# Performance work log

Hardware: AMD Instinct MI355X
Metric: run time of the kernel (lower is better)

The kernel has to match this reference:

```python
import jax, jax.numpy as jnp
import numpy as np

VOCAB = 20000
E = 300      # word embedding size (GloVe)
H = 1024     # n_hidden
G = 8        # n_head
N_OUT = 300  # output GloVe-space dim
N_ANS = 4000 # answer candidates
B, NQ, NK = 64, 32, 256


def setup_inputs() -> dict:
    key = jax.random.key(0)
    ks = jax.random.split(key, 12)
    s = lambda fan_in: 1.0 / np.sqrt(fan_in)
    return {
        "he_ques": jax.random.randint(ks[0], (B, NQ), 0, VOCAB),
        "he_kg": jax.random.randint(ks[1], (B, NK), 0, VOCAB),
        "emb": jax.random.normal(ks[2], (VOCAB, E), dtype=jnp.float32),
        "Wq": jax.random.normal(ks[3], (E, H), dtype=jnp.float32) * s(E),
        "bq": jnp.zeros((H,), dtype=jnp.float32),
        "Wk": jax.random.normal(ks[4], (E, H), dtype=jnp.float32) * s(E),
        "bk": jnp.zeros((H,), dtype=jnp.float32),
        "Watt": jax.random.normal(ks[5], (H, G), dtype=jnp.float32) * s(H),
        "batt": jnp.zeros((G,), dtype=jnp.float32),
        "Wout": jax.random.normal(ks[6], (H * G, N_OUT), dtype=jnp.float32) * s(H * G),
        "bout": jnp.zeros((N_OUT,), dtype=jnp.float32),
        "glove_cands": jax.random.normal(ks[7], (N_ANS, N_OUT), dtype=jnp.float32),
    }


def reference(he_ques, he_kg, emb, Wq, bq, Wk, bk, Watt, batt, Wout, bout, glove_cands):
    # Embed + project (dropout p=0 at eval)
    hq = emb[he_ques] @ Wq + bq          # [B, NQ, H]
    hk = emb[he_kg] @ Wk + bk            # [B, NK, H]
    # Attention logits: original builds outer product [B,NQ,NK,H] then Linear(H->G).
    # Fused as a single bilinear contraction (same math, no huge intermediate).
    logits = jnp.einsum('bqd,bkd,dg->bgqk', hq, hk, Watt) + batt[None, :, None, None]
    b, g, nq, nk = logits.shape
    att = jax.nn.softmax(logits.reshape(b, g, nq * nk), axis=2).reshape(b, g, nq, nk)
    # Per-head bilinear pooling: out[b,g,d] = sum_{q,k} hq[b,q,d] * att[b,g,q,k] * hk[b,k,d]
    pooled = jnp.einsum('bqd,bgqk,bkd->bgd', hq, att, hk)  # [B, G, H]
    out = pooled.reshape(b, g * hq.shape[-1]) @ Wout + bout  # [B, N_OUT]
    sim = out @ glove_cands.T                                # [B, N_ANS]
    return jax.nn.log_softmax(sim, axis=1)
```

## Files before the change

kernel.cpp:

```cpp
#include <hip/hip_runtime.h>
#include <math.h>

#define VOCAB 20000
#define E     300
#define EP    320
#define H     1024
#define G     8
#define NOUT  300
#define NP    320
#define KOUT  8192
#define NANS  4000
#define B     64
#define NQ    32
#define NK    256

typedef __attribute__((ext_vector_type(8))) short bf16x8;
typedef __attribute__((ext_vector_type(4))) float f32x4;

__device__ inline ushort f2bf(float x) {
    union { float f; unsigned u; } c; c.f = x;
    unsigned r = c.u + 0x7FFF + ((c.u >> 16) & 1);
    return (ushort)(r >> 16);
}
__device__ inline float bf2f(ushort x) {
    union { unsigned u; float f; } c; c.u = ((unsigned)x) << 16;
    return c.f;
}
#define MFMA(a, b, c) __builtin_amdgcn_mfma_f32_16x16x32_bf16((a), (b), (c), 0, 0, 0)

__global__ __launch_bounds__(256) void prep_emb(
    const float* __restrict__ emb, ushort* __restrict__ emb_bf)
{
    const int r0 = blockIdx.x * 64;
    for (int i = threadIdx.x; i < 64 * 80; i += 256) {
        int r = r0 + (i / 80), c = i % 80;
        if (r >= VOCAB) break;
        ushort4 o{0, 0, 0, 0};
        if (c < 75) {
            float4 v = *(const float4*)(emb + (long)r * E + c * 4);
            o.x = f2bf(v.x); o.y = f2bf(v.y); o.z = f2bf(v.z); o.w = f2bf(v.w);
        }
        *(ushort4*)(emb_bf + (long)r * EP + c * 4) = o;
    }
}

__global__ __launch_bounds__(256) void prep_wt(
    const float* __restrict__ Wq, const float* __restrict__ Wk,
    ushort* __restrict__ WTq, ushort* __restrict__ WTk)
{
    const float* W = blockIdx.z ? Wk : Wq;
    ushort* WT = blockIdx.z ? WTk : WTq;
    const int h0 = blockIdx.x * 64;
    const int e0 = blockIdx.y * 64;
    __shared__ float lf[64][65];
    const int t = threadIdx.x;

    for (int i = t; i < 64 * 64; i += 256) {
        int ec = i >> 6, hh = i & 63;
        int e = e0 + ec;
        lf[hh][ec] = (e < E) ? W[(long)e * H + h0 + hh] : 0.f;
    }
    __syncthreads();
    for (int i = t; i < 64 * 16; i += 256) {
        int hh = i >> 4, c = i & 15;
        ushort4 o;
        o.x = f2bf(lf[hh][c * 4 + 0]);
        o.y = f2bf(lf[hh][c * 4 + 1]);
        o.z = f2bf(lf[hh][c * 4 + 2]);
        o.w = f2bf(lf[hh][c * 4 + 3]);
        *(ushort4*)(WT + (long)(h0 + hh) * EP + e0 + c * 4) = o;
    }
}

__global__ __launch_bounds__(256) void prep_woutT(
    const float* __restrict__ Wout, ushort* __restrict__ woutT)
{
    const int k0 = blockIdx.x * 64, n0 = blockIdx.y * 64;
    __shared__ ushort td[64][72];
    for (int i = threadIdx.x; i < 64 * 64; i += 256) {
        int kk = i >> 6, nn = i & 63;
        int n = n0 + nn;
        float v = (n < NOUT) ? Wout[(k0 + kk) * NOUT + n] : 0.f;
        td[nn][kk] = f2bf(v);
    }
    __syncthreads();
    for (int i = threadIdx.x; i < 64 * 8; i += 256) {
        int nn = i >> 3, c = i & 7;
        *(bf16x8*)(woutT + (n0 + nn) * KOUT + k0 + c * 8) =
            *(const bf16x8*)(&td[nn][c * 8]);
    }
}

template <int WRITE_T>
__global__ __launch_bounds__(256, 2) void proj_big(
    const int* __restrict__ idx, const ushort* __restrict__ emb_bf,
    const ushort* __restrict__ WT, const float* __restrict__ bias,
    ushort* __restrict__ outr, ushort* __restrict__ outT)
{
    __shared__ ushort lds[128 * 130];
    __shared__ int sidx[128];
    const int r0 = blockIdx.x * 128;
    const int n0 = blockIdx.y * 128;
    const int t = threadIdx.x;

    if (t < 128) sidx[t] = idx[r0 + t];

    const int w = t >> 6, l = t & 63, lr = l & 15, lc = l >> 4;
    const int wm = (w >> 1) * 64, wn = (w & 1) * 64;
    const int srow = t >> 2;
    const int scol = (t & 3) * 8;
    ushort* As = lds;
    ushort* Bs = lds + 5120;
    f32x4 acc[4][4] = {};

    __syncthreads();

    for (int kk = 0; kk < 10; ++kk) {
        if (kk) __syncthreads();
        #pragma unroll
        for (int p = 0; p < 2; ++p) {
            int r = p * 64 + srow;
            *(bf16x8*)(As + r * 40 + scol) =
                *(const bf16x8*)(emb_bf + (long)sidx[r] * EP + kk * 32 + scol);
            *(bf16x8*)(Bs + r * 40 + scol) =
                *(const bf16x8*)(WT + (long)(n0 + r) * EP + kk * 32 + scol);
        }
        __syncthreads();

        bf16x8 af[4], bf[4];
        #pragma unroll
        for (int mf = 0; mf < 4; ++mf)
            af[mf] = *(const bf16x8*)(As + (wm + mf * 16 + lr) * 40 + lc * 8);
        #pragma unroll
        for (int nf = 0; nf < 4; ++nf)
            bf[nf] = *(const bf16x8*)(Bs + (wn + nf * 16 + lr) * 40 + lc * 8);
        #pragma unroll
        for (int mf = 0; mf < 4; ++mf)
            #pragma unroll
            for (int nf = 0; nf < 4; ++nf)
                acc[mf][nf] = MFMA(af[mf], bf[nf], acc[mf][nf]);
    }
    __syncthreads();

    #pragma unroll
    for (int mf = 0; mf < 4; ++mf)
    #pragma unroll
    for (int nf = 0; nf < 4; ++nf) {
        const int col = wn + nf * 16 + lr;
        const float bv = bias[n0 + col];
        #pragma unroll
        for (int r = 0; r < 4; ++r)
            lds[(wm + mf * 16 + lc * 4 + r) * 130 + col] =
                f2bf(acc[mf][nf][r] + bv);
    }
    __syncthreads();

    for (int i = t; i < 128 * 16; i += 256) {
        int k = i >> 4, c = i & 15;
        *(bf16x8*)(outr + (long)(r0 + k) * H + n0 + c * 8) =
            *(const bf16x8*)(lds + k * 130 + c * 8);
    }
    if (WRITE_T) {
        const int b = r0 >> 8, k0 = r0 & 255;
        for (int i = t; i < 128 * 16; i += 256) {
            int d = i >> 4, c = i & 15;
            ushort tmp[8];
            #pragma unroll
            for (int j = 0; j < 8; ++j) tmp[j] = lds[(c * 8 + j) * 130 + d];
            *(bf16x8*)(outT + (long)b * (H * NK) + (n0 + d) * NK + k0 + c * 8) =
                *(const bf16x8*)(tmp);
        }
    }
}

__global__ __launch_bounds__(512) void attn_mfma(
    const ushort* __restrict__ hq, const ushort* __restrict__ hk,
    const float* __restrict__ watt, const float* __restrict__ batt,
    ushort* __restrict__ att)
{
    const int b = blockIdx.x, g = blockIdx.y;
    const int t = threadIdx.x, w = t >> 6, l = t & 63, lr = l & 15, lc = l >> 4;
    __shared__ float wg[H];
    __shared__ ushort As[32 * 72];
    __shared__ ushort Bs[256 * 72];
    __shared__ float red[16];

    for (int i = t; i < H; i += 512) wg[i] = watt[i * G + g];

    f32x4 acc[2][2] = {};
    __syncthreads();

    for (int kk = 0; kk < 16; ++kk) {
        if (kk) __syncthreads();
        if (t < 256) {
            int r = t >> 3, c8 = (t & 7) * 8;
            bf16x8 hv = *(const bf16x8*)(hq + (b * NQ + r) * H + kk * 64 + c8);
            bf16x8 o;
            #pragma unroll
            for (int j = 0; j < 8; ++j)
                o[j] = (short)f2bf(bf2f((ushort)hv[j]) * wg[kk * 64 + c8 + j]);
            *(bf16x8*)(As + r * 72 + c8) = o;
        }
        #pragma unroll
        for (int p = 0; p < 4; ++p) {
            int j = t + 512 * p;
            int r = j >> 3, c8 = (j & 7) * 8;
            *(bf16x8*)(Bs + r * 72 + c8) =
                *(const bf16x8*)(hk + (b * NK + r) * H + kk * 64 + c8);
        }
        __syncthreads();

        #pragma unroll
        for (int ks = 0; ks < 2; ++ks) {
            bf16x8 a0 = *(const bf16x8*)(As + lr * 72 + ks * 32 + lc * 8);
            bf16x8 a1 = *(const bf16x8*)(As + (16 + lr) * 72 + ks * 32 + lc * 8);
            bf16x8 b0 = *(const bf16x8*)(Bs + (w * 32 + lr) * 72 + ks * 32 + lc * 8);
            bf16x8 b1 = *(const bf16x8*)(Bs + (w * 32 + 16 + lr) * 72 + ks * 32 + lc * 8);
            acc[0][0] = MFMA(a0, b0, acc[0][0]);
            acc[0][1] = MFMA(a0, b1, acc[0][1]);
            acc[1][0] = MFMA(a1, b0, acc[1][0]);
            acc[1][1] = MFMA(a1, b1, acc[1][1]);
        }
    }

    const float bg = batt[g];
    float lm = -1e30f;
    #pragma unroll
    for (int mt = 0; mt < 2; ++mt)
    #pragma unroll
    for (int nf = 0; nf < 2; ++nf)
    #pragma unroll
    for (int r = 0; r < 4; ++r) {
        acc[mt][nf][r] += bg;
        lm = fmaxf(lm, acc[mt][nf][r]);
    }
    #pragma unroll
    for (int off = 32; off; off >>= 1) lm = fmaxf(lm, __shfl_xor(lm, off));
    if (l == 0) red[w] = lm;
    __syncthreads();
    float gm = red[0];
    #pragma unroll
    for (int i = 1; i < 8; ++i) gm = fmaxf(gm, red[i]);

    float ls = 0.f;
    #pragma unroll
    for (int mt = 0; mt < 2; ++mt)
    #pragma unroll
    for (int nf = 0; nf < 2; ++nf)
    #pragma unroll
    for (int r = 0; r < 4; ++r) {
        float e = __expf(acc[mt][nf][r] - gm);
        acc[mt][nf][r] = e;
        ls += e;
    }
    #pragma unroll
    for (int off = 32; off; off >>= 1) ls += __shfl_xor(ls, off);
    if (l == 0) red[8 + w] = ls;
    __syncthreads();
    float sum = red[8];
    #pragma unroll
    for (int i = 9; i < 16; ++i) sum += red[i];
    const float inv = 1.f / sum;

    ushort* op = att + (b * 8 + g) * (NQ * NK);
    #pragma unroll
    for (int mt = 0; mt < 2; ++mt)
    #pragma unroll
    for (int nf = 0; nf < 2; ++nf)
    #pragma unroll
    for (int r = 0; r < 4; ++r)
        op[(mt * 16 + lc * 4 + r) * NK + w * 32 + nf * 16 + lr] =
            f2bf(acc[mt][nf][r] * inv);
}

__global__ __launch_bounds__(256, 2) void pooled_big(
    const ushort* __restrict__ att, const ushort* __restrict__ hkT,
    const ushort* __restrict__ hq, ushort* __restrict__ pooled_bf)
{
    __shared__ ushort lds[128 * 80];
    const int b = blockIdx.x, mt = blockIdx.y, nt = blockIdx.z;
    const int t = threadIdx.x;
    const int w = t >> 6, l = t & 63, lr = l & 15, lc = l >> 4;
    const int wm = (w >> 1) * 64, wn = (w & 1) * 64;
    const int srow = t >> 2;
    const int scol = (t & 3) * 8;
    ushort* As = lds;
    ushort* Bs = lds + 5120;
    const ushort* ab = att + (long)b * (G * NQ * NK) + (long)mt * 128 * NK;
    const ushort* bb = hkT + (long)b * (H * NK) + (long)nt * 128 * NK;
    f32x4 acc[4][4] = {};

    for (int kk = 0; kk < 8; ++kk) {
        if (kk) __syncthreads();
        #pragma unroll
        for (int p = 0; p < 2; ++p) {
            int r = p * 64 + srow;
            *(bf16x8*)(As + r * 40 + scol) =
                *(const bf16x8*)(ab + (long)r * NK + kk * 32 + scol);
            *(bf16x8*)(Bs + r * 40 + scol) =
                *(const bf16x8*)(bb + (long)r * NK + kk * 32 + scol);
        }
        __syncthreads();

        bf16x8 af[4], bf[4];
        #pragma unroll
        for (int mf = 0; mf < 4; ++mf)
            af[mf] = *(const bf16x8*)(As + (wm + mf * 16 + lr) * 40 + lc * 8);
        #pragma unroll
        for (int nf = 0; nf < 4; ++nf)
            bf[nf] = *(const bf16x8*)(Bs + (wn + nf * 16 + lr) * 40 + lc * 8);
        #pragma unroll
        for (int mf = 0; mf < 4; ++mf)
            #pragma unroll
            for (int nf = 0; nf < 4; ++nf)
                acc[mf][nf] = MFMA(af[mf], bf[nf], acc[mf][nf]);
    }
    __syncthreads();

    for (int i = t; i < 32 * 16; i += 256) {
        int r = i >> 4, c8 = (i & 15) * 8;
        *(bf16x8*)(lds + r * 136 + c8) =
            *(const bf16x8*)(hq + ((long)b * NQ + r) * H + nt * 128 + c8);
    }
    __syncthreads();

    float s[2][4] = {};
    #pragma unroll
    for (int nf = 0; nf < 4; ++nf) {
        const int col = wn + nf * 16 + lr;
        #pragma unroll
        for (int mf = 0; mf < 4; ++mf) {
            #pragma unroll
            for (int r = 0; r < 4; ++r) {
                const int q = (wm + mf * 16 + lc * 4 + r) & 31;
                s[mf >> 1][nf] += acc[mf][nf][r] * bf2f(lds[q * 136 + col]);
            }
        }
    }
    #pragma unroll
    for (int gl = 0; gl < 2; ++gl)
    #pragma unroll
    for (int nf = 0; nf < 4; ++nf) {
        float v = s[gl][nf];
        v += __shfl_xor(v, 16);
        v += __shfl_xor(v, 32);
        if (l < 16) {
            const int g = mt * 4 + (wm >> 5) + gl;
            const int d = nt * 128 + wn + nf * 16 + lr;
            pooled_bf[((long)b * G + g) * H + d] = f2bf(v);
        }
    }
}

__global__ __launch_bounds__(256) void outproj_mfma(
    const ushort* __restrict__ pooled_bf, const ushort* __restrict__ woutT,
    float* __restrict__ partial)
{
    const int ks = blockIdx.x;
    const int k0 = ks * 128;
    const int t = threadIdx.x, w = t >> 6, l = t & 63, lr = l & 15, lc = l >> 4;
    const ushort* ap = pooled_bf + lr * KOUT + k0 + lc * 8;
    const ushort* bp = woutT + (w * 80 + lr) * KOUT + k0 + lc * 8;
    f32x4 acc[4][5] = {};

    #pragma unroll
    for (int kk = 0; kk < 4; ++kk) {
        bf16x8 a[4];
        #pragma unroll
        for (int mt = 0; mt < 4; ++mt)
            a[mt] = *(const bf16x8*)(ap + mt * 16 * KOUT + kk * 32);
        #pragma unroll
        for (int nt = 0; nt < 5; ++nt) {
            bf16x8 bfr = *(const bf16x8*)(bp + nt * 16 * KOUT + kk * 32);
            #pragma unroll
            for (int mt = 0; mt < 4; ++mt)
                acc[mt][nt] = MFMA(a[mt], bfr, acc[mt][nt]);
        }
    }

    #pragma unroll
    for (int mt = 0; mt < 4; ++mt)
    #pragma unroll
    for (int nt = 0; nt < 5; ++nt)
    #pragma unroll
    for (int r = 0; r < 4; ++r) {
        const int bb = mt * 16 + lc * 4 + r;
        const int n = w * 80 + nt * 16 + lr;
        partial[(ks * B + bb) * NP + n] = acc[mt][nt][r];
    }
}

__global__ __launch_bounds__(256) void reduce_out_kernel(
    const float* __restrict__ partial, const float* __restrict__ bout,
    float* __restrict__ outv)
{
    const int i = blockIdx.x * 256 + threadIdx.x;
    if (i >= B * 304) return;
    const int b = i / 304, n = i % 304;
    float acc = 0.f;
    if (n < NOUT) {
        acc = bout[n];
        for (int ks = 0; ks < 64; ++ks)
            acc += partial[(ks * B + b) * NP + n];
    }
    outv[b * 304 + n] = acc;
}

__global__ __launch_bounds__(256) void sim_kernel(
    const float* __restrict__ outv, const float* __restrict__ glove,
    float* __restrict__ sim)
{
    __shared__ __align__(16) float ov[64][308];
    __shared__ __align__(16) float gl[16][308];
    const int t = threadIdx.x;
    const int a0 = blockIdx.x * 16;

    for (int i = t; i < 64 * 75; i += 256) {
        int r = i / 75, c = i % 75;
        *(float4*)(&ov[r][c * 4]) = *(const float4*)(&outv[r * 304 + c * 4]);
    }
    for (int i = t; i < 16 * 75; i += 256) {
        int r = i / 75, c = i % 75;
        *(float4*)(&gl[r][c * 4]) = *(const float4*)(&glove[(a0 + r) * NOUT + c * 4]);
    }
    __syncthreads();

    const int a = t & 15, bg = t >> 4;
    float acc[4] = {};
    for (int k4 = 0; k4 < 75; ++k4) {
        float4 g = *(const float4*)(&gl[a][k4 * 4]);
        #pragma unroll
        for (int bi = 0; bi < 4; ++bi) {
            float4 o = *(const float4*)(&ov[bg * 4 + bi][k4 * 4]);
            acc[bi] += g.x * o.x + g.y * o.y + g.z * o.z + g.w * o.w;
        }
    }
    #pragma unroll
    for (int bi = 0; bi < 4; ++bi)
        sim[(bg * 4 + bi) * NANS + a0 + a] = acc[bi];
}

__global__ __launch_bounds__(256) void lsm_kernel(
    const float* __restrict__ sim, float* __restrict__ dout)
{
    const int b = blockIdx.x, t = threadIdx.x;
    const float* p = sim + b * NANS;
    __shared__ float red[4];

    float4 v[4];
    float lm = -1e30f;
    #pragma unroll
    for (int j = 0; j < 4; ++j) {
        int i = t + j * 256;
        if (i < 1000) {
            v[j] = ((const float4*)p)[i];
            lm = fmaxf(lm, fmaxf(fmaxf(v[j].x, v[j].y), fmaxf(v[j].z, v[j].w)));
        }
    }
    #pragma unroll
    for (int off = 32; off; off >>= 1) lm = fmaxf(lm, __shfl_xor(lm, off));
    if ((t & 63) == 0) red[t >> 6] = lm;
    __syncthreads();
    const float gm = fmaxf(fmaxf(red[0], red[1]), fmaxf(red[2], red[3]));

    float ls = 0.f;
    #pragma unroll
    for (int j = 0; j < 4; ++j) {
        int i = t + j * 256;
        if (i < 1000)
            ls += __expf(v[j].x - gm) + __expf(v[j].y - gm) +
                  __expf(v[j].z - gm) + __expf(v[j].w - gm);
    }
    #pragma unroll
    for (int off = 32; off; off >>= 1) ls += __shfl_xor(ls, off);
    __syncthreads();
    if ((t & 63) == 0) red[t >> 6] = ls;
    __syncthreads();
    const float sh = gm + logf(red[0] + red[1] + red[2] + red[3]);

    #pragma unroll
    for (int j = 0; j < 4; ++j) {
        int i = t + j * 256;
        if (i < 1000) {
            float4 o;
            o.x = v[j].x - sh; o.y = v[j].y - sh;
            o.z = v[j].z - sh; o.w = v[j].w - sh;
            ((float4*)(dout + b * NANS))[i] = o;
        }
    }
}

extern "C" void kernel_launch(void* const* d_in, const int* in_sizes, int n_in,
                              void* d_out, int out_size, void* d_ws, size_t ws_size,
                              hipStream_t stream)
{
    (void)in_sizes; (void)n_in; (void)out_size; (void)ws_size;
    const int*   he_q  = (const int*)  d_in[0];
    const int*   he_k  = (const int*)  d_in[1];
    const float* emb   = (const float*)d_in[2];
    const float* Wq    = (const float*)d_in[3];
    const float* bq    = (const float*)d_in[4];
    const float* Wk    = (const float*)d_in[5];
    const float* bk    = (const float*)d_in[6];
    const float* Watt  = (const float*)d_in[7];
    const float* batt  = (const float*)d_in[8];
    const float* Wout  = (const float*)d_in[9];
    const float* bout  = (const float*)d_in[10];
    const float* glove = (const float*)d_in[11];
    float* out = (float*)d_out;

    ushort* WTq    = (ushort*)d_ws;
    ushort* WTk    = WTq + 327680;
    ushort* emb_bf = WTk + 327680;
    ushort* hq_bf  = emb_bf + 6400000;
    ushort* hk_bf  = hq_bf + 2097152;
    ushort* hkT    = hk_bf + 16777216;
    ushort* pool_bf= hkT + 16777216;
    ushort* woutT  = pool_bf + 524288;
    ushort* att    = woutT + 2621440;
    float*  partial= (float*)(att + 4194304);
    float*  outv   = partial + 1310720;
    float*  sim    = outv + 19456;

    prep_emb<<<dim3(313), 256, 0, stream>>>(emb, emb_bf);
    prep_wt<<<dim3(16, 5, 2), 256, 0, stream>>>(Wq, Wk, WTq, WTk);
    prep_woutT<<<dim3(128, 5), 256, 0, stream>>>(Wout, woutT);
    proj_big<0><<<dim3(16, 8), 256, 0, stream>>>(he_q, emb_bf, WTq, bq, hq_bf, nullptr);
    proj_big<1><<<dim3(128, 8), 256, 0, stream>>>(he_k, emb_bf, WTk, bk, hk_bf, hkT);
    attn_mfma<<<dim3(64, 8), 512, 0, stream>>>(hq_bf, hk_bf, Watt, batt, att);
    pooled_big<<<dim3(64, 2, 8), 256, 0, stream>>>(att, hkT, hq_bf, pool_bf);
    outproj_mfma<<<dim3(64), 256, 0, stream>>>(pool_bf, woutT, partial);
    reduce_out_kernel<<<dim3(76), 256, 0, stream>>>(partial, bout, outv);
    sim_kernel<<<dim3(250), 256, 0, stream>>>(outv, glove, sim);
    lsm_kernel<<<dim3(64), 256, 0, stream>>>(sim, out);
}
```

Before: 138.9 us.

## Gather fp32 embeddings directly in projection and merge prep/projection launches

```diff
diff --git a/kernel.cpp b/kernel.cpp
--- a/kernel.cpp
+++ b/kernel.cpp
@@ -28,78 +28,73 @@
 }
 #define MFMA(a, b, c) __builtin_amdgcn_mfma_f32_16x16x32_bf16((a), (b), (c), 0, 0, 0)
 
-__global__ __launch_bounds__(256) void prep_emb(
-    const float* __restrict__ emb, ushort* __restrict__ emb_bf)
-{
-    const int r0 = blockIdx.x * 64;
-    for (int i = threadIdx.x; i < 64 * 80; i += 256) {
-        int r = r0 + (i / 80), c = i % 80;
-        if (r >= VOCAB) break;
-        ushort4 o{0, 0, 0, 0};
-        if (c < 75) {
-            float4 v = *(const float4*)(emb + (long)r * E + c * 4);
-            o.x = f2bf(v.x); o.y = f2bf(v.y); o.z = f2bf(v.z); o.w = f2bf(v.w);
-        }
-        *(ushort4*)(emb_bf + (long)r * EP + c * 4) = o;
-    }
-}
-
-__global__ __launch_bounds__(256) void prep_wt(
+__global__ __launch_bounds__(256) void prep_weights(
     const float* __restrict__ Wq, const float* __restrict__ Wk,
-    ushort* __restrict__ WTq, ushort* __restrict__ WTk)
-{
-    const float* W = blockIdx.z ? Wk : Wq;
-    ushort* WT = blockIdx.z ? WTk : WTq;
-    const int h0 = blockIdx.x * 64;
-    const int e0 = blockIdx.y * 64;
-    __shared__ float lf[64][65];
+    const float* __restrict__ Wout,
+    ushort* __restrict__ WTq, ushort* __restrict__ WTk,
+    ushort* __restrict__ woutT)
+{
+    __shared__ __align__(16) float lf[64 * 65];
+    const int id = blockIdx.x;
     const int t = threadIdx.x;
 
-    for (int i = t; i < 64 * 64; i += 256) {
-        int ec = i >> 6, hh = i & 63;
-        int e = e0 + ec;
-        lf[hh][ec] = (e < E) ? W[(long)e * H + h0 + hh] : 0.f;
-    }
-    __syncthreads();
-    for (int i = t; i < 64 * 16; i += 256) {
-        int hh = i >> 4, c = i & 15;
-        ushort4 o;
-        o.x = f2bf(lf[hh][c * 4 + 0]);
-        o.y = f2bf(lf[hh][c * 4 + 1]);
-        o.z = f2bf(lf[hh][c * 4 + 2]);
-        o.w = f2bf(lf[hh][c * 4 + 3]);
-        *(ushort4*)(WT + (long)(h0 + hh) * EP + e0 + c * 4) = o;
-    }
-}
-
-__global__ __launch_bounds__(256) void prep_woutT(
-    const float* __restrict__ Wout, ushort* __restrict__ woutT)
-{
-    const int k0 = blockIdx.x * 64, n0 = blockIdx.y * 64;
-    __shared__ ushort td[64][72];
-    for (int i = threadIdx.x; i < 64 * 64; i += 256) {
-        int kk = i >> 6, nn = i & 63;
-        int n = n0 + nn;
-        float v = (n < NOUT) ? Wout[(k0 + kk) * NOUT + n] : 0.f;
-        td[nn][kk] = f2bf(v);
-    }
-    __syncthreads();
-    for (int i = threadIdx.x; i < 64 * 8; i += 256) {
-        int nn = i >> 3, c = i & 7;
-        *(bf16x8*)(woutT + (n0 + nn) * KOUT + k0 + c * 8) =
-            *(const bf16x8*)(&td[nn][c * 8]);
-    }
-}
-
-template <int WRITE_T>
-__global__ __launch_bounds__(256, 2) void proj_big(
-    const int* __restrict__ idx, const ushort* __restrict__ emb_bf,
-    const ushort* __restrict__ WT, const float* __restrict__ bias,
-    ushort* __restrict__ outr, ushort* __restrict__ outT)
+    if (id < 160) {
+        const int hT = id % 16, eT = (id / 16) % 5, z = id / 80;
+        const float* W = z ? Wk : Wq;
+        ushort* WT = z ? WTk : WTq;
+        const int h0 = hT * 64, e0 = eT * 64;
+
+        for (int i = t; i < 64 * 64; i += 256) {
+            int ec = i >> 6, hh = i & 63;
+            int e = e0 + ec;
+            lf[hh * 65 + ec] = (e < E) ? W[(long)e * H + h0 + hh] : 0.f;
+        }
+        __syncthreads();
+        for (int i = t; i < 64 * 16; i += 256) {
+            int hh = i >> 4, c = i & 15;
+            ushort4 o;
+            o.x = f2bf(lf[hh * 65 + c * 4 + 0]);
+            o.y = f2bf(lf[hh * 65 + c * 4 + 1]);
+            o.z = f2bf(lf[hh * 65 + c * 4 + 2]);
+            o.w = f2bf(lf[hh * 65 + c * 4 + 3]);
+            *(ushort4*)(WT + (long)(h0 + hh) * EP + e0 + c * 4) = o;
+        }
+    } else {
+        ushort* td = (ushort*)lf;
+        const int wid = id - 160;
+        const int k0 = (wid & 127) * 64, n0 = (wid >> 7) * 64;
+        for (int i = t; i < 64 * 64; i += 256) {
+            int kk = i >> 6, nn = i & 63;
+            int n = n0 + nn;
+            float v = (n < NOUT) ? Wout[(long)(k0 + kk) * NOUT + n] : 0.f;
+            td[nn * 72 + kk] = f2bf(v);
+        }
+        __syncthreads();
+        for (int i = t; i < 64 * 8; i += 256) {
+            int nn = i >> 3, c = i & 7;
+            *(bf16x8*)(woutT + (long)(n0 + nn) * KOUT + k0 + c * 8) =
+                *(const bf16x8*)(&td[nn * 72 + c * 8]);
+        }
+    }
+}
+
+__global__ __launch_bounds__(256, 2) void proj_all(
+    const int* __restrict__ he_q, const int* __restrict__ he_k,
+    const float* __restrict__ emb,
+    const ushort* __restrict__ WTq, const ushort* __restrict__ WTk,
+    const float* __restrict__ bq, const float* __restrict__ bk,
+    ushort* __restrict__ hq_bf, ushort* __restrict__ hk_bf,
+    ushort* __restrict__ hkT)
 {
     __shared__ ushort lds[128 * 130];
     __shared__ int sidx[128];
-    const int r0 = blockIdx.x * 128;
+    const bool isq = blockIdx.x < 16;
+    const int xt = isq ? blockIdx.x : blockIdx.x - 16;
+    const int* __restrict__ idx = isq ? he_q : he_k;
+    const ushort* __restrict__ WT = isq ? WTq : WTk;
+    const float* __restrict__ bias = isq ? bq : bk;
+    ushort* __restrict__ outr = isq ? hq_bf : hk_bf;
+    const int r0 = xt * 128;
     const int n0 = blockIdx.y * 128;
     const int t = threadIdx.x;
 
@@ -117,11 +112,25 @@
 
     for (int kk = 0; kk < 10; ++kk) {
         if (kk) __syncthreads();
+        const int e0 = kk * 32 + scol;
         #pragma unroll
         for (int p = 0; p < 2; ++p) {
             int r = p * 64 + srow;
-            *(bf16x8*)(As + r * 40 + scol) =
-                *(const bf16x8*)(emb_bf + (long)sidx[r] * EP + kk * 32 + scol);
+            const float* src = emb + (long)sidx[r] * E;
+            bf16x8 o;
+            if (e0 + 8 <= E) {
+                float4 v0 = *(const float4*)(src + e0);
+                float4 v1 = *(const float4*)(src + e0 + 4);
+                o[0] = (short)f2bf(v0.x); o[1] = (short)f2bf(v0.y);
+                o[2] = (short)f2bf(v0.z); o[3] = (short)f2bf(v0.w);
+                o[4] = (short)f2bf(v1.x); o[5] = (short)f2bf(v1.y);
+                o[6] = (short)f2bf(v1.z); o[7] = (short)f2bf(v1.w);
+            } else {
+                #pragma unroll
+                for (int j = 0; j < 8; ++j)
+                    o[j] = (short)f2bf((e0 + j < E) ? src[e0 + j] : 0.f);
+            }
+            *(bf16x8*)(As + r * 40 + scol) = o;
             *(bf16x8*)(Bs + r * 40 + scol) =
                 *(const bf16x8*)(WT + (long)(n0 + r) * EP + kk * 32 + scol);
         }
@@ -160,14 +169,14 @@
         *(bf16x8*)(outr + (long)(r0 + k) * H + n0 + c * 8) =
             *(const bf16x8*)(lds + k * 130 + c * 8);
     }
-    if (WRITE_T) {
+    if (!isq) {
         const int b = r0 >> 8, k0 = r0 & 255;
         for (int i = t; i < 128 * 16; i += 256) {
             int d = i >> 4, c = i & 15;
             ushort tmp[8];
             #pragma unroll
             for (int j = 0; j < 8; ++j) tmp[j] = lds[(c * 8 + j) * 130 + d];
-            *(bf16x8*)(outT + (long)b * (H * NK) + (n0 + d) * NK + k0 + c * 8) =
+            *(bf16x8*)(hkT + (long)b * (H * NK) + (n0 + d) * NK + k0 + c * 8) =
                 *(const bf16x8*)(tmp);
         }
     }
@@ -511,8 +520,7 @@
 
     ushort* WTq    = (ushort*)d_ws;
     ushort* WTk    = WTq + 327680;
-    ushort* emb_bf = WTk + 327680;
-    ushort* hq_bf  = emb_bf + 6400000;
+    ushort* hq_bf  = WTk + 327680;
     ushort* hk_bf  = hq_bf + 2097152;
     ushort* hkT    = hk_bf + 16777216;
     ushort* pool_bf= hkT + 16777216;
@@ -522,11 +530,9 @@
     float*  outv   = partial + 1310720;
     float*  sim    = outv + 19456;
 
-    prep_emb<<<dim3(313), 256, 0, stream>>>(emb, emb_bf);
-    prep_wt<<<dim3(16, 5, 2), 256, 0, stream>>>(Wq, Wk, WTq, WTk);
-    prep_woutT<<<dim3(128, 5), 256, 0, stream>>>(Wout, woutT);
-    proj_big<0><<<dim3(16, 8), 256, 0, stream>>>(he_q, emb_bf, WTq, bq, hq_bf, nullptr);
-    proj_big<1><<<dim3(128, 8), 256, 0, stream>>>(he_k, emb_bf, WTk, bk, hk_bf, hkT);
+    prep_weights<<<dim3(800), 256, 0, stream>>>(Wq, Wk, Wout, WTq, WTk, woutT);
+    proj_all<<<dim3(144, 8), 256, 0, stream>>>(he_q, he_k, emb, WTq, WTk,
+                                               bq, bk, hq_bf, hk_bf, hkT);
     attn_mfma<<<dim3(64, 8), 512, 0, stream>>>(hq_bf, hk_bf, Watt, batt, att);
     pooled_big<<<dim3(64, 2, 8), 256, 0, stream>>>(att, hkT, hq_bf, pool_bf);
     outproj_mfma<<<dim3(64), 256, 0, stream>>>(pool_bf, woutT, partial);
```

Result: faster. 129.4 us (-6.9%).
